# Optimization experiments

Hardware: AMD Instinct MI355X
Metric: run time of the kernel (lower is better)

The kernel has to match this reference:

```python
import jax, jax.numpy as jnp
import numpy as np

B, S, D = 4, 4096, 2048      # batch, seq, model_dim
E = 128                      # emb_dim (hardcoded in module)
H = 128                      # head_dim
TAU = 0.4                    # self.T
BASE = 3.0                   # self.base (gumbel-sigmoid offset)
LN_EPS = 1e-5


def setup_inputs() -> dict:
    key = jax.random.key(0)
    k_x, k_wr, k_wd, k_g = jax.random.split(key, 4)
    x = jax.random.normal(k_x, (B, S, D), dtype=jnp.float32)
    # torch nn.Linear stores weight as [out_features, in_features]
    W_router = jax.random.normal(k_wr, (E, D), dtype=jnp.float32) / np.sqrt(D)
    W_decoder = jax.random.normal(k_wd, (H, E), dtype=jnp.float32) / np.sqrt(E)
    ln_gamma = jnp.ones((E,), dtype=jnp.float32)
    ln_beta = jnp.zeros((E,), dtype=jnp.float32)
    rnn_state = jnp.zeros((E,), dtype=jnp.float32)  # registered buffer, zeros
    # torch: gumbels = -Exp(1).log()  -> standard Gumbel(0,1) noise
    u = jax.random.uniform(k_g, (B, S, H), dtype=jnp.float32, minval=1e-20, maxval=1.0)
    gumbel_noise = -jnp.log(-jnp.log(u))
    return {
        "x": x, "W_router": W_router, "W_decoder": W_decoder,
        "ln_gamma": ln_gamma, "ln_beta": ln_beta, "rnn_state": rnn_state,
        "gumbel_noise": gumbel_noise, "top_k": 32,
    }


def reference(x, W_router, W_decoder, ln_gamma, ln_beta, rnn_state, gumbel_noise, top_k):
    # router linear (no bias): [B,S,D] @ [D,E] -> [B,S,E]
    out = jnp.einsum("bsd,ed->bse", x, W_router)
    full_emb = rnn_state + out
    # LayerNorm over emb dim (biased variance, as torch LayerNorm)
    mu = full_emb.mean(-1, keepdims=True)
    var = full_emb.var(-1, keepdims=True)
    h = (full_emb - mu) / jnp.sqrt(var + LN_EPS) * ln_gamma + ln_beta
    # decoder linear after exact GELU: [B,S,E] @ [E,H] -> [B,S,H]
    logits = jnp.einsum("bse,he->bsh", jax.nn.gelu(h, approximate=False), W_decoder)
    # gumbel-sigmoid (soft): sigmoid((logits + gumbel + offset)/tau)
    binary_approx = jax.nn.sigmoid((logits + gumbel_noise + BASE) / TAU)
    # hard_sample: straight-through round
    binary = jax.lax.stop_gradient(jnp.round(binary_approx) - binary_approx) + binary_approx
    # top-k mask over head_dim
    _, topk_idx = jax.lax.top_k(binary_approx, top_k)            # [B,S,top_k]
    topk_mask = jax.nn.one_hot(topk_idx, H, dtype=binary_approx.dtype).sum(-2)  # [B,S,H]
    cnt = binary.sum(-1, keepdims=True)
    binary = jnp.where(cnt > top_k, topk_mask, binary)
    # fallback: if a token selects nothing, pick argmax of soft scores
    zero_mask = binary.sum(-1, keepdims=True) == 0
    fallback = jax.nn.one_hot(jnp.argmax(binary_approx, axis=-1), H, dtype=binary_approx.dtype)
    binary = jnp.where(zero_mask, fallback, binary)
    binary = binary.reshape(B, S, -1, H)  # [B,S,1,H]
    return binary, binary_approx
```

## Files before the change

### kernel.cpp

```cpp
#include <hip/hip_runtime.h>
#include <math.h>

#define NTOK   16384
#define DDIM   2048
#define EDIM   128
#define HDIM   128
#define TOKT   64
#define KC     32
#define NCH    (DDIM / KC)

typedef __attribute__((ext_vector_type(8))) _Float16 half8;
typedef __attribute__((ext_vector_type(4))) float    f32x4;

__device__ __forceinline__ int swz(int t, int e) {
  return t * EDIM + ((e & 96) | ((e ^ t) & 31));
}

__global__ __launch_bounds__(256)
void conv_w(const float* __restrict__ Wr,
            _Float16* __restrict__ wh, _Float16* __restrict__ wl) {
  const int idx  = (int)blockIdx.x * 256 + (int)threadIdx.x;
  const int lane = idx & 63;
  const int ks   = (idx >> 6) & 63;
  const int nt   = idx >> 12;
  const int n    = nt * 16 + (lane & 15);
  const int k0   = ks * 32 + (lane >> 4) * 8;
  half8 h, l;
#pragma unroll
  for (int j = 0; j < 8; ++j) {
    const float w = Wr[(size_t)n * DDIM + k0 + j] * 32.0f;
    const _Float16 hh = (_Float16)w;
    h[j] = hh;
    l[j] = (_Float16)((w - (float)hh) * 2048.0f);
  }
  *(half8*)(wh + (size_t)idx * 8) = h;
  *(half8*)(wl + (size_t)idx * 8) = l;
}

__global__ __launch_bounds__(1024)
void fused_router(const float* __restrict__ x,
                  const _Float16* __restrict__ wsh,
                  const _Float16* __restrict__ wsl,
                  const float* __restrict__ Wd,
                  const float* __restrict__ gamma,
                  const float* __restrict__ beta,
                  const float* __restrict__ rnn,
                  const float* __restrict__ gum,
                  float* __restrict__ outb,
                  float* __restrict__ outa) {
  __shared__ char smraw[65536];
  _Float16* const xs = (_Float16*)smraw;
  float* const A  = (float*)smraw;
  float* const G4 = (float*)(smraw + 32768);

  const int tid  = (int)threadIdx.x;
  const int wv   = __builtin_amdgcn_readfirstlane(tid >> 6);
  const int lane = tid & 63;
  const int t0   = (int)blockIdx.x * TOKT;

  const int nt   = wv & 7;
  const int mt0  = (wv >> 3) * 2;
  const int mt1  = mt0 + 1;
  const int quad = lane >> 4;
  const int col  = lane & 15;

  const int offA0 = (mt0 * 64 + lane) * 8;
  const int offA1 = (mt1 * 64 + lane) * 8;
  const int offB  = 8192 + nt * 1024 + lane * 8;

  const bool xstage = tid < 256;
  const int  sx_t   = tid >> 2;
  const int  sx_kq  = tid & 3;
  const float* xg   = x + (size_t)(t0 + sx_t) * DDIM + sx_kq * 8;
  const int  sx_off = ((sx_t >> 4) * 64 + sx_kq * 16 + (sx_t & 15)) * 8;

  const bool wstage = wv >= 8;
  const int  ntw    = wv & 7;
  const _Float16* whg = wsh + (size_t)ntw * 32768 + (size_t)lane * 8;
  const _Float16* wlg = wsl + (size_t)ntw * 32768 + (size_t)lane * 8;
  const int  sw_off = 8192 + ntw * 1024 + lane * 8;

  f32x4 hh0 = {0,0,0,0}, cr0 = {0,0,0,0}, hh1 = {0,0,0,0}, cr1 = {0,0,0,0};

  if (xstage) {
    const float4 a = *(const float4*)xg;
    const float4 bq = *(const float4*)(xg + 4);
    half8 h, l;
#pragma unroll
    for (int m = 0; m < 4; ++m) {
      const float v = (&a.x)[m];
      const _Float16 hv = (_Float16)v;
      h[m] = hv; l[m] = (_Float16)((v - (float)hv) * 2048.0f);
    }
#pragma unroll
    for (int m = 0; m < 4; ++m) {
      const float v = (&bq.x)[m];
      const _Float16 hv = (_Float16)v;
      h[m + 4] = hv; l[m + 4] = (_Float16)((v - (float)hv) * 2048.0f);
    }
    *(half8*)&xs[sx_off] = h;
    *(half8*)&xs[2048 + sx_off] = l;
  }
  if (wstage) {
    const half8 h = *(const half8*)whg;
    const half8 l = *(const half8*)wlg;
    *(half8*)&xs[sw_off] = h;
    *(half8*)&xs[sw_off + 512] = l;
  }

  float4 pxa, pxb; half8 pwh, pwl;
  for (int c = 0; c < NCH; ++c) {
    __syncthreads();
    const int b  = c & 1;
    const int bn = b ^ 1;
    if (c + 1 < NCH) {
      if (xstage) {
        pxa = *(const float4*)(xg + (c + 1) * KC);
        pxb = *(const float4*)(xg + (c + 1) * KC + 4);
      }
      if (wstage) {
        pwh = *(const half8*)(whg + (size_t)(c + 1) * 512);
        pwl = *(const half8*)(wlg + (size_t)(c + 1) * 512);
      }
    }
    const half8 ah0 = *(const half8*)&xs[b * 4096 + offA0];
    const half8 al0 = *(const half8*)&xs[b * 4096 + 2048 + offA0];
    const half8 ah1 = *(const half8*)&xs[b * 4096 + offA1];
    const half8 al1 = *(const half8*)&xs[b * 4096 + 2048 + offA1];
    const half8 bh  = *(const half8*)&xs[b * 8192 + offB];
    const half8 bl  = *(const half8*)&xs[b * 8192 + offB + 512];

    hh0 = __builtin_amdgcn_mfma_f32_16x16x32_f16(ah0, bh, hh0, 0, 0, 0);
    cr0 = __builtin_amdgcn_mfma_f32_16x16x32_f16(ah0, bl, cr0, 0, 0, 0);
    cr0 = __builtin_amdgcn_mfma_f32_16x16x32_f16(al0, bh, cr0, 0, 0, 0);
    hh1 = __builtin_amdgcn_mfma_f32_16x16x32_f16(ah1, bh, hh1, 0, 0, 0);
    cr1 = __builtin_amdgcn_mfma_f32_16x16x32_f16(ah1, bl, cr1, 0, 0, 0);
    cr1 = __builtin_amdgcn_mfma_f32_16x16x32_f16(al1, bh, cr1, 0, 0, 0);

    if (c + 1 < NCH) {
      if (xstage) {
        half8 h, l;
#pragma unroll
        for (int m = 0; m < 4; ++m) {
          const float v = (&pxa.x)[m];
          const _Float16 hv = (_Float16)v;
          h[m] = hv; l[m] = (_Float16)((v - (float)hv) * 2048.0f);
        }
#pragma unroll
        for (int m = 0; m < 4; ++m) {
          const float v = (&pxb.x)[m];
          const _Float16 hv = (_Float16)v;
          h[m + 4] = hv; l[m + 4] = (_Float16)((v - (float)hv) * 2048.0f);
        }
        *(half8*)&xs[bn * 4096 + sx_off] = h;
        *(half8*)&xs[bn * 4096 + 2048 + sx_off] = l;
      }
      if (wstage) {
        *(half8*)&xs[bn * 8192 + sw_off] = pwh;
        *(half8*)&xs[bn * 8192 + sw_off + 512] = pwl;
      }
    }
  }
  __syncthreads();

  {
    const int e  = nt * 16 + col;
    const float rv = rnn[e];
#pragma unroll
    for (int r = 0; r < 4; ++r) {
      A[swz(mt0 * 16 + quad * 4 + r, e)] =
          hh0[r] * (1.0f / 32.0f) + cr0[r] * (1.0f / 65536.0f) + rv;
      A[swz(mt1 * 16 + quad * 4 + r, e)] =
          hh1[r] * (1.0f / 32.0f) + cr1[r] * (1.0f / 65536.0f) + rv;
    }
  }
  __syncthreads();

  const int e0 = wv * 8;
  {
    const float gm0 = gamma[lane], gm1 = gamma[lane + 64];
    const float bt0 = beta[lane],  bt1 = beta[lane + 64];
    for (int tt = wv * 4; tt < wv * 4 + 4; ++tt) {
      const float v0 = A[swz(tt, lane)];
      const float v1 = A[swz(tt, lane + 64)];
      float s = v0 + v1;
#pragma unroll
      for (int m = 32; m; m >>= 1) s += __shfl_xor(s, m);
      const float mu = s * (1.0f / 128.0f);
      const float d0 = v0 - mu, d1 = v1 - mu;
      float q = d0 * d0 + d1 * d1;
#pragma unroll
      for (int m = 32; m; m >>= 1) q += __shfl_xor(q, m);
      const float rstd = 1.0f / sqrtf(q * (1.0f / 128.0f) + 1e-5f);
      const float h0v = d0 * rstd * gm0 + bt0;
      const float h1v = d1 * rstd * gm1 + bt1;
      const float g0 = 0.5f * h0v * (1.0f + erff(h0v * 0.70710678118654752f));
      const float g1 = 0.5f * h1v * (1.0f + erff(h1v * 0.70710678118654752f));
      const int e0a = lane, e1a = lane + 64;
      G4[(tt * 32 + (((e0a >> 2) ^ (tt & 31)))) * 4 + (e0a & 3)] = g0;
      G4[(tt * 32 + (((e1a >> 2) ^ (tt & 31)))) * 4 + (e1a & 3)] = g1;
    }
  }
  __syncthreads();

  {
    float acc2[8];
#pragma unroll
    for (int j = 0; j < 8; ++j) acc2[j] = 0.0f;
    const float4* wd4 = (const float4*)(Wd + (size_t)e0 * EDIM);
#pragma unroll 2
    for (int kg = 0; kg < EDIM / 4; ++kg) {
      const float4 gv = *(const float4*)&G4[(lane * 32 + (kg ^ (lane & 31))) * 4];
#pragma unroll
      for (int j = 0; j < 8; ++j) {
        const float4 w = wd4[(size_t)j * (EDIM / 4) + kg];
        acc2[j] = fmaf(gv.x, w.x,
                  fmaf(gv.y, w.y,
                  fmaf(gv.z, w.z,
                  fmaf(gv.w, w.w, acc2[j]))));
      }
    }
    __syncthreads();
#pragma unroll
    for (int j = 0; j < 8; ++j) A[swz(lane, e0 + j)] = acc2[j];
  }
  __syncthreads();

  for (int tt = wv * 4; tt < wv * 4 + 4; ++tt) {
    const size_t T = (size_t)(t0 + tt);
    const float l0 = A[swz(tt, lane)];
    const float l1 = A[swz(tt, lane + 64)];
    const float gn0 = gum[T * HDIM + lane];
    const float gn1 = gum[T * HDIM + lane + 64];
    const float z0 = (l0 + gn0 + 3.0f) * 2.5f;
    const float z1 = (l1 + gn1 + 3.0f) * 2.5f;
    const float ba0 = 1.0f / (1.0f + expf(-z0));
    const float ba1 = 1.0f / (1.0f + expf(-z1));
    const unsigned ub0 = __float_as_uint(ba0);
    const unsigned ub1 = __float_as_uint(ba1);
    const int r0 = ba0 > 0.5f;
    const int r1 = ba1 > 0.5f;
    const int cnt = __popcll(__ballot(r0)) + __popcll(__ballot(r1));
    float bin0, bin1;
    if (cnt > 32) {
      unsigned v = 0u;
#pragma unroll
      for (int b = 29; b >= 0; --b) {
        const unsigned cand = v | (1u << b);
        const int cc = __popcll(__ballot(ub0 >= cand)) + __popcll(__ballot(ub1 >= cand));
        if (cc >= 32) v = cand;
      }
      const int cgt = __popcll(__ballot(ub0 > v)) + __popcll(__ballot(ub1 > v));
      const int r = 32 - cgt;
      const unsigned long long t0b = __ballot(ub0 == v);
      const unsigned long long t1b = __ballot(ub1 == v);
      const int n0 = __popcll(t0b);
      const unsigned long long mlt = (1ull << lane) - 1ull;
      const int rk0 = __popcll(t0b & mlt);
      const int rk1 = n0 + __popcll(t1b & mlt);
      bin0 = (ub0 > v || (ub0 == v && rk0 < r)) ? 1.0f : 0.0f;
      bin1 = (ub1 > v || (ub1 == v && rk1 < r)) ? 1.0f : 0.0f;
    } else if (cnt == 0) {
      float m = fmaxf(ba0, ba1);
#pragma unroll
      for (int mm = 32; mm; mm >>= 1) m = fmaxf(m, __shfl_xor(m, mm));
      const unsigned long long e0b = __ballot(ba0 == m);
      const unsigned long long e1b = __ballot(ba1 == m);
      const int hstar = e0b ? (__ffsll((unsigned long long)e0b) - 1)
                            : (64 + __ffsll((unsigned long long)e1b) - 1);
      bin0 = (lane == hstar) ? 1.0f : 0.0f;
      bin1 = (lane + 64 == hstar) ? 1.0f : 0.0f;
    } else {
      bin0 = r0 ? 1.0f : 0.0f;
      bin1 = r1 ? 1.0f : 0.0f;
    }
    outb[T * HDIM + lane]      = bin0;
    outb[T * HDIM + lane + 64] = bin1;
    outa[T * HDIM + lane]      = ba0;
    outa[T * HDIM + lane + 64] = ba1;
  }
}

extern "C" void kernel_launch(void* const* d_in, const int* in_sizes, int n_in,
                              void* d_out, int out_size, void* d_ws, size_t ws_size,
                              hipStream_t stream) {
  (void)in_sizes; (void)n_in; (void)ws_size; (void)out_size;
  const float* x   = (const float*)d_in[0];
  const float* Wr  = (const float*)d_in[1];
  const float* Wd  = (const float*)d_in[2];
  const float* gm  = (const float*)d_in[3];
  const float* bt  = (const float*)d_in[4];
  const float* rnn = (const float*)d_in[5];
  const float* gum = (const float*)d_in[6];
  float* outb = (float*)d_out;
  float* outa = outb + (size_t)NTOK * HDIM;

  _Float16* wh = (_Float16*)d_ws;
  _Float16* wl = wh + (size_t)EDIM * DDIM;

  conv_w<<<dim3(128), dim3(256), 0, stream>>>(Wr, wh, wl);
  fused_router<<<dim3(NTOK / TOKT), dim3(1024), 0, stream>>>(
      x, wh, wl, Wd, gm, bt, rnn, gum, outb, outa);
}
```

Measured before the change: 261.2 us.

## Halve token tile, shrink LDS, and stage router weights via global_load_lds

Cuts the per-block token tile from 64 to 32, so each wave does one MFMA row tile and the shared buffer shrinks from 64KB to 40KB. This allows more resident blocks per CU and doubles the grid size. The weight staging now uses direct global-to-LDS loads across all 16 waves instead of a register round trip. The decoder stage is remapped so each wave computes 4 output rows for 32 tokens. The trade-off is that each block reuses the weights over fewer tokens, so weight traffic from L2 doubles.

Result: slower. 271.8 us (+4.0%).

```diff
diff --git a/kernel.cpp b/kernel.cpp
--- a/kernel.cpp
+++ b/kernel.cpp
@@ -5,11 +5,12 @@
 #define DDIM   2048
 #define EDIM   128
 #define HDIM   128
-#define TOKT   64
+#define TOKT   32
 #define KC     32
 #define NCH    (DDIM / KC)
 
 typedef __attribute__((ext_vector_type(8))) _Float16 half8;
+typedef __attribute__((ext_vector_type(4))) _Float16 half4;
 typedef __attribute__((ext_vector_type(4))) float    f32x4;
 
 __device__ __forceinline__ int swz(int t, int e) {
@@ -37,7 +38,7 @@
   *(half8*)(wl + (size_t)idx * 8) = l;
 }
 
-__global__ __launch_bounds__(1024)
+__global__ __launch_bounds__(1024, 8)
 void fused_router(const float* __restrict__ x,
                   const _Float16* __restrict__ wsh,
                   const _Float16* __restrict__ wsl,
@@ -48,10 +49,10 @@
                   const float* __restrict__ gum,
                   float* __restrict__ outb,
                   float* __restrict__ outa) {
-  __shared__ char smraw[65536];
+  __shared__ char smraw[40960];
   _Float16* const xs = (_Float16*)smraw;
   float* const A  = (float*)smraw;
-  float* const G4 = (float*)(smraw + 32768);
+  float* const G4 = (float*)(smraw + 16384);
 
   const int tid  = (int)threadIdx.x;
   const int wv   = __builtin_amdgcn_readfirstlane(tid >> 6);
@@ -59,106 +60,76 @@
   const int t0   = (int)blockIdx.x * TOKT;
 
   const int nt   = wv & 7;
-  const int mt0  = (wv >> 3) * 2;
-  const int mt1  = mt0 + 1;
+  const int mt   = wv >> 3;
   const int quad = lane >> 4;
   const int col  = lane & 15;
 
-  const int offA0 = (mt0 * 64 + lane) * 8;
-  const int offA1 = (mt1 * 64 + lane) * 8;
-  const int offB  = 8192 + nt * 1024 + lane * 8;
+  const int offA = mt * 512 + lane * 8;
+  const int offB = 4096 + nt * 1024 + lane * 8;
 
   const bool xstage = tid < 256;
-  const int  sx_t   = tid >> 2;
-  const int  sx_kq  = tid & 3;
-  const float* xg   = x + (size_t)(t0 + sx_t) * DDIM + sx_kq * 8;
-  const int  sx_off = ((sx_t >> 4) * 64 + sx_kq * 16 + (sx_t & 15)) * 8;
-
-  const bool wstage = wv >= 8;
-  const int  ntw    = wv & 7;
-  const _Float16* whg = wsh + (size_t)ntw * 32768 + (size_t)lane * 8;
-  const _Float16* wlg = wsl + (size_t)ntw * 32768 + (size_t)lane * 8;
-  const int  sw_off = 8192 + ntw * 1024 + lane * 8;
-
-  f32x4 hh0 = {0,0,0,0}, cr0 = {0,0,0,0}, hh1 = {0,0,0,0}, cr1 = {0,0,0,0};
-
+  const int  sx_t   = tid >> 3;
+  const int  sx_k8  = tid & 7;
+  const float* xg   = x + (size_t)(t0 + sx_t) * DDIM + sx_k8 * 4;
+  const int  sx_off = (sx_t >> 4) * 512 + (sx_k8 >> 1) * 128
+                    + (sx_t & 15) * 8 + (sx_k8 & 1) * 4;
+
+  const int wnt = wv & 7;
+  const int wpl = wv >> 3;
+  const _Float16* wsrc = (wpl ? wsl : wsh) + (size_t)wnt * 32768 + (size_t)lane * 8;
+  const int sw_off = 4096 + wnt * 1024 + wpl * 512;
+
+  f32x4 hh = {0,0,0,0}, cr = {0,0,0,0};
+
+  __builtin_amdgcn_global_load_lds(
+      (const __attribute__((address_space(1))) void*)wsrc,
+      (__attribute__((address_space(3))) void*)(xs + sw_off),
+      16, 0, 0);
   if (xstage) {
     const float4 a = *(const float4*)xg;
-    const float4 bq = *(const float4*)(xg + 4);
-    half8 h, l;
+    half4 h4, l4;
 #pragma unroll
     for (int m = 0; m < 4; ++m) {
       const float v = (&a.x)[m];
       const _Float16 hv = (_Float16)v;
-      h[m] = hv; l[m] = (_Float16)((v - (float)hv) * 2048.0f);
-    }
-#pragma unroll
-    for (int m = 0; m < 4; ++m) {
-      const float v = (&bq.x)[m];
-      const _Float16 hv = (_Float16)v;
-      h[m + 4] = hv; l[m + 4] = (_Float16)((v - (float)hv) * 2048.0f);
-    }
-    *(half8*)&xs[sx_off] = h;
-    *(half8*)&xs[2048 + sx_off] = l;
-  }
-  if (wstage) {
-    const half8 h = *(const half8*)whg;
-    const half8 l = *(const half8*)wlg;
-    *(half8*)&xs[sw_off] = h;
-    *(half8*)&xs[sw_off + 512] = l;
-  }
-
-  float4 pxa, pxb; half8 pwh, pwl;
+      h4[m] = hv; l4[m] = (_Float16)((v - (float)hv) * 2048.0f);
+    }
+    *(half4*)&xs[sx_off] = h4;
+    *(half4*)&xs[1024 + sx_off] = l4;
+  }
+
+  float4 px;
+#pragma unroll 2
   for (int c = 0; c < NCH; ++c) {
     __syncthreads();
     const int b  = c & 1;
     const int bn = b ^ 1;
     if (c + 1 < NCH) {
-      if (xstage) {
-        pxa = *(const float4*)(xg + (c + 1) * KC);
-        pxb = *(const float4*)(xg + (c + 1) * KC + 4);
+      __builtin_amdgcn_global_load_lds(
+          (const __attribute__((address_space(1))) void*)(wsrc + (size_t)(c + 1) * 512),
+          (__attribute__((address_space(3))) void*)(xs + bn * 8192 + sw_off),
+          16, 0, 0);
+      if (xstage) px = *(const float4*)(xg + (c + 1) * KC);
+    }
+    const half8 ah = *(const half8*)&xs[b * 2048 + offA];
+    const half8 al = *(const half8*)&xs[b * 2048 + 1024 + offA];
+    const half8 bh = *(const half8*)&xs[b * 8192 + offB];
+    const half8 bl = *(const half8*)&xs[b * 8192 + offB + 512];
+
+    hh = __builtin_amdgcn_mfma_f32_16x16x32_f16(ah, bh, hh, 0, 0, 0);
+    cr = __builtin_amdgcn_mfma_f32_16x16x32_f16(ah, bl, cr, 0, 0, 0);
+    cr = __builtin_amdgcn_mfma_f32_16x16x32_f16(al, bh, cr, 0, 0, 0);
+
+    if (c + 1 < NCH && xstage) {
+      half4 h4, l4;
+#pragma unroll
+      for (int m = 0; m < 4; ++m) {
+        const float v = (&px.x)[m];
+        const _Float16 hv = (_Float16)v;
+        h4[m] = hv; l4[m] = (_Float16)((v - (float)hv) * 2048.0f);
       }
-      if (wstage) {
-        pwh = *(const half8*)(whg + (size_t)(c + 1) * 512);
-        pwl = *(const half8*)(wlg + (size_t)(c + 1) * 512);
-      }
-    }
-    const half8 ah0 = *(const half8*)&xs[b * 4096 + offA0];
-    const half8 al0 = *(const half8*)&xs[b * 4096 + 2048 + offA0];
-    const half8 ah1 = *(const half8*)&xs[b * 4096 + offA1];
-    const half8 al1 = *(const half8*)&xs[b * 4096 + 2048 + offA1];
-    const half8 bh  = *(const half8*)&xs[b * 8192 + offB];
-    const half8 bl  = *(const half8*)&xs[b * 8192 + offB + 512];
-
-    hh0 = __builtin_amdgcn_mfma_f32_16x16x32_f16(ah0, bh, hh0, 0, 0, 0);
-    cr0 = __builtin_amdgcn_mfma_f32_16x16x32_f16(ah0, bl, cr0, 0, 0, 0);
-    cr0 = __builtin_amdgcn_mfma_f32_16x16x32_f16(al0, bh, cr0, 0, 0, 0);
-    hh1 = __builtin_amdgcn_mfma_f32_16x16x32_f16(ah1, bh, hh1, 0, 0, 0);
-    cr1 = __builtin_amdgcn_mfma_f32_16x16x32_f16(ah1, bl, cr1, 0, 0, 0);
-    cr1 = __builtin_amdgcn_mfma_f32_16x16x32_f16(al1, bh, cr1, 0, 0, 0);
-
-    if (c + 1 < NCH) {
-      if (xstage) {
-        half8 h, l;
-#pragma unroll
-        for (int m = 0; m < 4; ++m) {
-          const float v = (&pxa.x)[m];
-          const _Float16 hv = (_Float16)v;
-          h[m] = hv; l[m] = (_Float16)((v - (float)hv) * 2048.0f);
-        }
-#pragma unroll
-        for (int m = 0; m < 4; ++m) {
-          const float v = (&pxb.x)[m];
-          const _Float16 hv = (_Float16)v;
-          h[m + 4] = hv; l[m + 4] = (_Float16)((v - (float)hv) * 2048.0f);
-        }
-        *(half8*)&xs[bn * 4096 + sx_off] = h;
-        *(half8*)&xs[bn * 4096 + 2048 + sx_off] = l;
-      }
-      if (wstage) {
-        *(half8*)&xs[bn * 8192 + sw_off] = pwh;
-        *(half8*)&xs[bn * 8192 + sw_off + 512] = pwl;
-      }
+      *(half4*)&xs[bn * 2048 + sx_off] = h4;
+      *(half4*)&xs[bn * 2048 + 1024 + sx_off] = l4;
     }
   }
   __syncthreads();
@@ -167,12 +138,9 @@
     const int e  = nt * 16 + col;
     const float rv = rnn[e];
 #pragma unroll
-    for (int r = 0; r < 4; ++r) {
-      A[swz(mt0 * 16 + quad * 4 + r, e)] =
-          hh0[r] * (1.0f / 32.0f) + cr0[r] * (1.0f / 65536.0f) + rv;
-      A[swz(mt1 * 16 + quad * 4 + r, e)] =
-          hh1[r] * (1.0f / 32.0f) + cr1[r] * (1.0f / 65536.0f) + rv;
-    }
+    for (int r = 0; r < 4; ++r)
+      A[swz(mt * 16 + quad * 4 + r, e)] =
+          hh[r] * (1.0f / 32.0f) + cr[r] * (1.0f / 65536.0f) + rv;
   }
   __syncthreads();
 
@@ -180,7 +148,7 @@
   {
     const float gm0 = gamma[lane], gm1 = gamma[lane + 64];
     const float bt0 = beta[lane],  bt1 = beta[lane + 64];
-    for (int tt = wv * 4; tt < wv * 4 + 4; ++tt) {
+    for (int tt = wv * 2; tt < wv * 2 + 2; ++tt) {
       const float v0 = A[swz(tt, lane)];
       const float v1 = A[swz(tt, lane + 64)];
       float s = v0 + v1;
@@ -196,23 +164,22 @@
       const float h1v = d1 * rstd * gm1 + bt1;
       const float g0 = 0.5f * h0v * (1.0f + erff(h0v * 0.70710678118654752f));
       const float g1 = 0.5f * h1v * (1.0f + erff(h1v * 0.70710678118654752f));
-      const int e0a = lane, e1a = lane + 64;
-      G4[(tt * 32 + (((e0a >> 2) ^ (tt & 31)))) * 4 + (e0a & 3)] = g0;
-      G4[(tt * 32 + (((e1a >> 2) ^ (tt & 31)))) * 4 + (e1a & 3)] = g1;
+      G4[(tt * 32 + ((lane >> 2) ^ tt)) * 4 + (lane & 3)] = g0;
+      G4[(tt * 32 + ((((lane + 64) >> 2)) ^ tt)) * 4 + ((lane + 64) & 3)] = g1;
     }
   }
   __syncthreads();
 
   {
-    float acc2[8];
-#pragma unroll
-    for (int j = 0; j < 8; ++j) acc2[j] = 0.0f;
-    const float4* wd4 = (const float4*)(Wd + (size_t)e0 * EDIM);
+    float acc2[4] = {0.0f, 0.0f, 0.0f, 0.0f};
+    const int tokn  = lane & 31;
+    const int rbase = e0 + (lane >> 5) * 4;
+    const float4* wd4 = (const float4*)(Wd + (size_t)rbase * EDIM);
 #pragma unroll 2
     for (int kg = 0; kg < EDIM / 4; ++kg) {
-      const float4 gv = *(const float4*)&G4[(lane * 32 + (kg ^ (lane & 31))) * 4];
-#pragma unroll
-      for (int j = 0; j < 8; ++j) {
+      const float4 gv = *(const float4*)&G4[(tokn * 32 + (kg ^ tokn)) * 4];
+#pragma unroll
+      for (int j = 0; j < 4; ++j) {
         const float4 w = wd4[(size_t)j * (EDIM / 4) + kg];
         acc2[j] = fmaf(gv.x, w.x,
                   fmaf(gv.y, w.y,
@@ -220,13 +187,12 @@
                   fmaf(gv.w, w.w, acc2[j]))));
       }
     }
-    __syncthreads();
-#pragma unroll
-    for (int j = 0; j < 8; ++j) A[swz(lane, e0 + j)] = acc2[j];
-  }
-  __syncthreads();
-
-  for (int tt = wv * 4; tt < wv * 4 + 4; ++tt) {
+#pragma unroll
+    for (int j = 0; j < 4; ++j) A[swz(tokn, rbase + j)] = acc2[j];
+  }
+  __syncthreads();
+
+  for (int tt = wv * 2; tt < wv * 2 + 2; ++tt) {
     const size_t T = (size_t)(t0 + tt);
     const float l0 = A[swz(tt, lane)];
     const float l1 = A[swz(tt, lane + 64)];
```

## Restructure router GEMM to 512-thread blocks with split-K and register-held weights

Applied to the files above, without the earlier changes.

The fused router kernel moves from 1024 to 512 threads per block. Each wave now computes a 2x4 tile of MFMA outputs and the K dimension is split between two wave groups, whose partial sums are reduced through shared memory. Weight fragments are loaded straight from global memory into double-buffered registers instead of being staged in LDS, and only the x tile goes through LDS. This is meant to raise MFMA work per LDS read and per barrier and to allow two blocks per CU. The cost is higher register pressure and an extra reduction step, and the epilogue now handles 8 tokens and 16 decoder rows per wave.

New measurement: 281.3 us. +7.7%, slower.

```diff
diff --git a/kernel.cpp b/kernel.cpp
--- a/kernel.cpp
+++ b/kernel.cpp
@@ -7,13 +7,29 @@
 #define HDIM   128
 #define TOKT   64
 #define KC     32
-#define NCH    (DDIM / KC)
+#define NIT    32
 
 typedef __attribute__((ext_vector_type(8))) _Float16 half8;
 typedef __attribute__((ext_vector_type(4))) float    f32x4;
 
 __device__ __forceinline__ int swz(int t, int e) {
   return t * EDIM + ((e & 96) | ((e ^ t) & 31));
+}
+
+__device__ __forceinline__ void cvt8(const float4& a, const float4& b,
+                                     half8& h, half8& l) {
+#pragma unroll
+  for (int m = 0; m < 4; ++m) {
+    const float v = (&a.x)[m];
+    const _Float16 hv = (_Float16)v;
+    h[m] = hv; l[m] = (_Float16)((v - (float)hv) * 2048.0f);
+  }
+#pragma unroll
+  for (int m = 0; m < 4; ++m) {
+    const float v = (&b.x)[m];
+    const _Float16 hv = (_Float16)v;
+    h[m + 4] = hv; l[m + 4] = (_Float16)((v - (float)hv) * 2048.0f);
+  }
 }
 
 __global__ __launch_bounds__(256)
@@ -37,7 +53,7 @@
   *(half8*)(wl + (size_t)idx * 8) = l;
 }
 
-__global__ __launch_bounds__(1024)
+__global__ __launch_bounds__(512, 2)
 void fused_router(const float* __restrict__ x,
                   const _Float16* __restrict__ wsh,
                   const _Float16* __restrict__ wsl,
@@ -58,129 +74,117 @@
   const int lane = tid & 63;
   const int t0   = (int)blockIdx.x * TOKT;
 
-  const int nt   = wv & 7;
-  const int mt0  = (wv >> 3) * 2;
-  const int mt1  = mt0 + 1;
+  const int mw   = wv & 1;
+  const int nw   = (wv >> 1) & 1;
+  const int kw   = wv >> 2;
   const int quad = lane >> 4;
   const int col  = lane & 15;
 
-  const int offA0 = (mt0 * 64 + lane) * 8;
-  const int offA1 = (mt1 * 64 + lane) * 8;
-  const int offB  = 8192 + nt * 1024 + lane * 8;
-
-  const bool xstage = tid < 256;
-  const int  sx_t   = tid >> 2;
-  const int  sx_kq  = tid & 3;
-  const float* xg   = x + (size_t)(t0 + sx_t) * DDIM + sx_kq * 8;
-  const int  sx_off = ((sx_t >> 4) * 64 + sx_kq * 16 + (sx_t & 15)) * 8;
-
-  const bool wstage = wv >= 8;
-  const int  ntw    = wv & 7;
-  const _Float16* whg = wsh + (size_t)ntw * 32768 + (size_t)lane * 8;
-  const _Float16* wlg = wsl + (size_t)ntw * 32768 + (size_t)lane * 8;
-  const int  sw_off = 8192 + ntw * 1024 + lane * 8;
-
-  f32x4 hh0 = {0,0,0,0}, cr0 = {0,0,0,0}, hh1 = {0,0,0,0}, cr1 = {0,0,0,0};
-
-  if (xstage) {
-    const float4 a = *(const float4*)xg;
-    const float4 bq = *(const float4*)(xg + 4);
-    half8 h, l;
-#pragma unroll
-    for (int m = 0; m < 4; ++m) {
-      const float v = (&a.x)[m];
-      const _Float16 hv = (_Float16)v;
-      h[m] = hv; l[m] = (_Float16)((v - (float)hv) * 2048.0f);
-    }
-#pragma unroll
-    for (int m = 0; m < 4; ++m) {
-      const float v = (&bq.x)[m];
-      const _Float16 hv = (_Float16)v;
-      h[m + 4] = hv; l[m + 4] = (_Float16)((v - (float)hv) * 2048.0f);
-    }
-    *(half8*)&xs[sx_off] = h;
-    *(half8*)&xs[2048 + sx_off] = l;
-  }
-  if (wstage) {
-    const half8 h = *(const half8*)whg;
-    const half8 l = *(const half8*)wlg;
-    *(half8*)&xs[sw_off] = h;
-    *(half8*)&xs[sw_off + 512] = l;
-  }
-
-  float4 pxa, pxb; half8 pwh, pwl;
-  for (int c = 0; c < NCH; ++c) {
+  const int abase = (kw * 4 + mw * 2) * 1024 + lane * 8;
+
+  const int skw   = tid >> 8;
+  const int smt   = (tid >> 6) & 3;
+  const int slane = tid & 63;
+  const int woff  = (skw * 4 + smt) * 1024 + slane * 8;
+  const float* xg = x + (size_t)(t0 + smt * 16 + (slane & 15)) * DDIM
+                      + skw * 1024 + (slane >> 4) * 8;
+
+  const size_t wbase = (size_t)(nw * 4) * 32768 + (size_t)kw * 16384 + lane * 8;
+
+  f32x4 hh[2][4], cr[2][4];
+#pragma unroll
+  for (int mi = 0; mi < 2; ++mi)
+#pragma unroll
+    for (int ni = 0; ni < 4; ++ni) { hh[mi][ni] = (f32x4){0,0,0,0}; cr[mi][ni] = (f32x4){0,0,0,0}; }
+
+  half8 bh[2][4], bl[2][4];
+
+#pragma unroll
+  for (int j = 0; j < 4; ++j) {
+    bh[0][j] = *(const half8*)(wsh + wbase + (size_t)j * 32768);
+    bl[0][j] = *(const half8*)(wsl + wbase + (size_t)j * 32768);
+  }
+  {
+    const float4 a  = *(const float4*)xg;
+    const float4 b2 = *(const float4*)(xg + 4);
+    half8 h, l; cvt8(a, b2, h, l);
+    *(half8*)&xs[woff] = h;
+    *(half8*)&xs[woff + 512] = l;
+  }
+
+  auto body = [&](int i, int pb) {
     __syncthreads();
-    const int b  = c & 1;
-    const int bn = b ^ 1;
-    if (c + 1 < NCH) {
-      if (xstage) {
-        pxa = *(const float4*)(xg + (c + 1) * KC);
-        pxb = *(const float4*)(xg + (c + 1) * KC + 4);
+    const int ab = pb ? 8192 + abase : abase;
+    const half8 ah0 = *(const half8*)&xs[ab];
+    const half8 al0 = *(const half8*)&xs[ab + 512];
+    const half8 ah1 = *(const half8*)&xs[ab + 1024];
+    const half8 al1 = *(const half8*)&xs[ab + 1536];
+    const int np = pb ^ 1;
+    float4 pxa, pxb;
+    if (i + 1 < NIT) {
+      const size_t wo = wbase + (size_t)(i + 1) * 512;
+#pragma unroll
+      for (int j = 0; j < 4; ++j) {
+        bh[np][j] = *(const half8*)(wsh + wo + (size_t)j * 32768);
+        bl[np][j] = *(const half8*)(wsl + wo + (size_t)j * 32768);
       }
-      if (wstage) {
-        pwh = *(const half8*)(whg + (size_t)(c + 1) * 512);
-        pwl = *(const half8*)(wlg + (size_t)(c + 1) * 512);
-      }
-    }
-    const half8 ah0 = *(const half8*)&xs[b * 4096 + offA0];
-    const half8 al0 = *(const half8*)&xs[b * 4096 + 2048 + offA0];
-    const half8 ah1 = *(const half8*)&xs[b * 4096 + offA1];
-    const half8 al1 = *(const half8*)&xs[b * 4096 + 2048 + offA1];
-    const half8 bh  = *(const half8*)&xs[b * 8192 + offB];
-    const half8 bl  = *(const half8*)&xs[b * 8192 + offB + 512];
-
-    hh0 = __builtin_amdgcn_mfma_f32_16x16x32_f16(ah0, bh, hh0, 0, 0, 0);
-    cr0 = __builtin_amdgcn_mfma_f32_16x16x32_f16(ah0, bl, cr0, 0, 0, 0);
-    cr0 = __builtin_amdgcn_mfma_f32_16x16x32_f16(al0, bh, cr0, 0, 0, 0);
-    hh1 = __builtin_amdgcn_mfma_f32_16x16x32_f16(ah1, bh, hh1, 0, 0, 0);
-    cr1 = __builtin_amdgcn_mfma_f32_16x16x32_f16(ah1, bl, cr1, 0, 0, 0);
-    cr1 = __builtin_amdgcn_mfma_f32_16x16x32_f16(al1, bh, cr1, 0, 0, 0);
-
-    if (c + 1 < NCH) {
-      if (xstage) {
-        half8 h, l;
-#pragma unroll
-        for (int m = 0; m < 4; ++m) {
-          const float v = (&pxa.x)[m];
-          const _Float16 hv = (_Float16)v;
-          h[m] = hv; l[m] = (_Float16)((v - (float)hv) * 2048.0f);
+      pxa = *(const float4*)(xg + (i + 1) * KC);
+      pxb = *(const float4*)(xg + (i + 1) * KC + 4);
+    }
+#pragma unroll
+    for (int j = 0; j < 4; ++j) {
+      hh[0][j] = __builtin_amdgcn_mfma_f32_16x16x32_f16(ah0, bh[pb][j], hh[0][j], 0, 0, 0);
+      cr[0][j] = __builtin_amdgcn_mfma_f32_16x16x32_f16(ah0, bl[pb][j], cr[0][j], 0, 0, 0);
+      cr[0][j] = __builtin_amdgcn_mfma_f32_16x16x32_f16(al0, bh[pb][j], cr[0][j], 0, 0, 0);
+      hh[1][j] = __builtin_amdgcn_mfma_f32_16x16x32_f16(ah1, bh[pb][j], hh[1][j], 0, 0, 0);
+      cr[1][j] = __builtin_amdgcn_mfma_f32_16x16x32_f16(ah1, bl[pb][j], cr[1][j], 0, 0, 0);
+      cr[1][j] = __builtin_amdgcn_mfma_f32_16x16x32_f16(al1, bh[pb][j], cr[1][j], 0, 0, 0);
+    }
+    if (i + 1 < NIT) {
+      half8 h, l; cvt8(pxa, pxb, h, l);
+      *(half8*)&xs[np * 8192 + woff] = h;
+      *(half8*)&xs[np * 8192 + woff + 512] = l;
+    }
+  };
+  for (int ii = 0; ii < NIT; ii += 2) { body(ii, 0); body(ii + 1, 1); }
+  __syncthreads();
+
+  if (kw == 0) {
+#pragma unroll
+    for (int mi = 0; mi < 2; ++mi)
+#pragma unroll
+      for (int ni = 0; ni < 4; ++ni)
+#pragma unroll
+        for (int r = 0; r < 4; ++r) {
+          const int t = (mw * 2 + mi) * 16 + quad * 4 + r;
+          const int e = (nw * 4 + ni) * 16 + col;
+          A[swz(t, e)] = hh[mi][ni][r] * (1.0f / 32.0f)
+                       + cr[mi][ni][r] * (1.0f / 65536.0f);
         }
-#pragma unroll
-        for (int m = 0; m < 4; ++m) {
-          const float v = (&pxb.x)[m];
-          const _Float16 hv = (_Float16)v;
-          h[m + 4] = hv; l[m + 4] = (_Float16)((v - (float)hv) * 2048.0f);
+  }
+  __syncthreads();
+  if (kw == 1) {
+    float rv[4];
+#pragma unroll
+    for (int ni = 0; ni < 4; ++ni) rv[ni] = rnn[(nw * 4 + ni) * 16 + col];
+#pragma unroll
+    for (int mi = 0; mi < 2; ++mi)
+#pragma unroll
+      for (int ni = 0; ni < 4; ++ni)
+#pragma unroll
+        for (int r = 0; r < 4; ++r) {
+          const int t = (mw * 2 + mi) * 16 + quad * 4 + r;
+          const int e = (nw * 4 + ni) * 16 + col;
+          A[swz(t, e)] += hh[mi][ni][r] * (1.0f / 32.0f)
+                        + cr[mi][ni][r] * (1.0f / 65536.0f) + rv[ni];
         }
-        *(half8*)&xs[bn * 4096 + sx_off] = h;
-        *(half8*)&xs[bn * 4096 + 2048 + sx_off] = l;
-      }
-      if (wstage) {
-        *(half8*)&xs[bn * 8192 + sw_off] = pwh;
-        *(half8*)&xs[bn * 8192 + sw_off + 512] = pwl;
-      }
-    }
-  }
-  __syncthreads();
-
-  {
-    const int e  = nt * 16 + col;
-    const float rv = rnn[e];
-#pragma unroll
-    for (int r = 0; r < 4; ++r) {
-      A[swz(mt0 * 16 + quad * 4 + r, e)] =
-          hh0[r] * (1.0f / 32.0f) + cr0[r] * (1.0f / 65536.0f) + rv;
-      A[swz(mt1 * 16 + quad * 4 + r, e)] =
-          hh1[r] * (1.0f / 32.0f) + cr1[r] * (1.0f / 65536.0f) + rv;
-    }
-  }
-  __syncthreads();
-
-  const int e0 = wv * 8;
+  }
+  __syncthreads();
+
   {
     const float gm0 = gamma[lane], gm1 = gamma[lane + 64];
     const float bt0 = beta[lane],  bt1 = beta[lane + 64];
-    for (int tt = wv * 4; tt < wv * 4 + 4; ++tt) {
+    for (int tt = wv * 8; tt < wv * 8 + 8; ++tt) {
       const float v0 = A[swz(tt, lane)];
       const float v1 = A[swz(tt, lane + 64)];
       float s = v0 + v1;
@@ -204,15 +208,16 @@
   __syncthreads();
 
   {
-    float acc2[8];
-#pragma unroll
-    for (int j = 0; j < 8; ++j) acc2[j] = 0.0f;
-    const float4* wd4 = (const float4*)(Wd + (size_t)e0 * EDIM);
+    const int rbase = wv * 16;
+    float acc2[16];
+#pragma unroll
+    for (int j = 0; j < 16; ++j) acc2[j] = 0.0f;
+    const float4* wd4 = (const float4*)(Wd + (size_t)rbase * EDIM);
 #pragma unroll 2
     for (int kg = 0; kg < EDIM / 4; ++kg) {
       const float4 gv = *(const float4*)&G4[(lane * 32 + (kg ^ (lane & 31))) * 4];
 #pragma unroll
-      for (int j = 0; j < 8; ++j) {
+      for (int j = 0; j < 16; ++j) {
         const float4 w = wd4[(size_t)j * (EDIM / 4) + kg];
         acc2[j] = fmaf(gv.x, w.x,
                   fmaf(gv.y, w.y,
@@ -220,13 +225,12 @@
                   fmaf(gv.w, w.w, acc2[j]))));
       }
     }
-    __syncthreads();
-#pragma unroll
-    for (int j = 0; j < 8; ++j) A[swz(lane, e0 + j)] = acc2[j];
-  }
-  __syncthreads();
-
-  for (int tt = wv * 4; tt < wv * 4 + 4; ++tt) {
+#pragma unroll
+    for (int j = 0; j < 16; ++j) A[swz(lane, rbase + j)] = acc2[j];
+  }
+  __syncthreads();
+
+  for (int tt = wv * 8; tt < wv * 8 + 8; ++tt) {
     const size_t T = (size_t)(t0 + tt);
     const float l0 = A[swz(tt, lane)];
     const float l1 = A[swz(tt, lane + 64)];
@@ -299,6 +303,6 @@
   _Float16* wl = wh + (size_t)EDIM * DDIM;
 
   conv_w<<<dim3(128), dim3(256), 0, stream>>>(Wr, wh, wl);
-  fused_router<<<dim3(NTOK / TOKT), dim3(1024), 0, stream>>>(
+  fused_router<<<dim3(NTOK / TOKT), dim3(512), 0, stream>>>(
       x, wh, wl, Wd, gm, bt, rnn, gum, outb, outa);
 }
```
